# Performance work log

Hardware: AMD Instinct MI355X
Metric: run time of the kernel (lower is better)

Reference implementation:

```python
import jax, jax.numpy as jnp
import numpy as np

NUM_HEADS = 16
HEIGHT = 32
WIDTH = 32
FEATURES_DIM = HEIGHT * WIDTH  # 1024
EMBED_DIM = 1024


def setup_inputs() -> dict:
    key = jax.random.key(0)
    ks = jax.random.split(key, 9)
    s_in = 1.0 / np.sqrt(FEATURES_DIM)
    s_e = 1.0 / np.sqrt(EMBED_DIM)
    return {
        "x": jax.random.normal(ks[0], (16, 512, HEIGHT, WIDTH), dtype=jnp.float32),
        "Wq": jax.random.uniform(ks[1], (EMBED_DIM, FEATURES_DIM), jnp.float32, -s_in, s_in),
        "bq": jax.random.uniform(ks[2], (EMBED_DIM,), jnp.float32, -s_in, s_in),
        "Wk": jax.random.uniform(ks[3], (EMBED_DIM, FEATURES_DIM), jnp.float32, -s_in, s_in),
        "bk": jax.random.uniform(ks[4], (EMBED_DIM,), jnp.float32, -s_in, s_in),
        "Wv": jax.random.uniform(ks[5], (EMBED_DIM, FEATURES_DIM), jnp.float32, -s_in, s_in),
        "bv": jax.random.uniform(ks[6], (EMBED_DIM,), jnp.float32, -s_in, s_in),
        "Wo": jax.random.uniform(ks[7], (FEATURES_DIM, EMBED_DIM), jnp.float32, -s_e, s_e),
        "bo": jax.random.uniform(ks[8], (FEATURES_DIM,), jnp.float32, -s_e, s_e),
    }


def reference(x, Wq, bq, Wk, bk, Wv, bv, Wo, bo):
    B, C, H, W = x.shape
    nh = NUM_HEADS
    hd = EMBED_DIM // nh
    xf = x.reshape(B, C, H * W)  # [B, C, F] - channel tokens
    q = xf @ Wq.T + bq  # [B, C, E]
    k = xf @ Wk.T + bk
    v = xf @ Wv.T + bv
    q = q.reshape(B, C, nh, hd).transpose(0, 2, 1, 3)  # [B, nh, C, hd]
    k = k.reshape(B, C, nh, hd).transpose(0, 2, 1, 3)
    v = v.reshape(B, C, nh, hd).transpose(0, 2, 1, 3)
    scores = jnp.einsum("bhcd,bhkd->bhck", q, k) / jnp.sqrt(jnp.float32(hd))
    attn = jax.nn.softmax(scores, axis=-1)
    out = jnp.einsum("bhck,bhkd->bhcd", attn, v)  # [B, nh, C, hd]
    out = out.transpose(0, 2, 1, 3).reshape(B, C, EMBED_DIM)
    out = out @ Wo.T + bo  # [B, C, F]
    return out.reshape(B, C, H, W)
```

## Files before the change

kernel.cpp:

```cpp
#include <hip/hip_runtime.h>


typedef unsigned short u16;
typedef __attribute__((ext_vector_type(8))) short short8;
typedef __attribute__((ext_vector_type(4))) float f32x4;
typedef __attribute__((ext_vector_type(4))) unsigned short u16x4;

#define MFMA16(a, b, c) __builtin_amdgcn_mfma_f32_16x16x32_bf16(a, b, c, 0, 0, 0)

__device__ __forceinline__ u16 f2bf(float x) {
  unsigned u = __float_as_uint(x);
  u += 0x7FFFu + ((u >> 16) & 1u);
  return (u16)(u >> 16);
}

__device__ __forceinline__ void async16(const void* g, void* l) {
  __builtin_amdgcn_global_load_lds(
      (__attribute__((address_space(1))) unsigned int*)(g),
      (__attribute__((address_space(3))) unsigned int*)(l), 16, 0, 0);
}

__global__ __launch_bounds__(256) void cvt_all(
    const float* __restrict__ x, const float* __restrict__ wq,
    const float* __restrict__ wk, const float* __restrict__ wv,
    const float* __restrict__ wo, u16* __restrict__ dst) {
  int g = blockIdx.x * 256 + threadIdx.x;
  const float* s;
  int off;
  if (g < 2097152) {
    s = x; off = g;
  } else {
    int r = g - 2097152;
    int w = r >> 18;
    off = r & 262143;
    s = (w == 0) ? wq : (w == 1) ? wk : (w == 2) ? wv : wo;
  }
  f32x4 v = ((const f32x4*)s)[off];
  u16x4 o;
#pragma unroll
  for (int j = 0; j < 4; ++j) o[j] = f2bf(v[j]);
  ((u16x4*)dst)[g] = o;
}

__device__ __forceinline__ void gemm8p(const u16* __restrict__ A,
                                       const u16* __restrict__ W, int m0,
                                       int n0, u16* lds, f32x4 acc[8][4]) {
  const int t = threadIdx.x;
  const int wave = t >> 6, lane = t & 63, lr = lane & 15, lg = lane >> 4;
  const int wr = wave >> 2, wn = wave & 3;
  const int srow = t >> 3;
  const int scol = ((t & 7) ^ (srow & 7)) << 3;
  const u16* gA = A + (size_t)(m0 + srow) * 1024 + scol;
  const u16* gB = W + (size_t)(n0 + srow) * 1024 + scol;
  u16* stA = lds + wave * 512;
  u16* stB = lds + 16384 + wave * 512;
  const int arow = (wr * 128 + lr) * 64;
  const int brow = 16384 + (wn * 64 + lr) * 64;
  const int xk = lr & 7;
  const int sw0 = (lg ^ xk) << 3;
  const int sw1 = ((4 + lg) ^ xk) << 3;

#define SA(kt, h)                                                           \
  {                                                                         \
    async16(gA + (2 * (h)) * 65536 + (kt) * 64,                             \
            stA + ((kt) & 1) * 32768 + (2 * (h)) * 4096);                   \
    async16(gA + (2 * (h) + 1) * 65536 + (kt) * 64,                         \
            stA + ((kt) & 1) * 32768 + (2 * (h) + 1) * 4096);               \
  }
#define SB(kt, h)                                                           \
  {                                                                         \
    async16(gB + (2 * (h)) * 65536 + (kt) * 64,                             \
            stB + ((kt) & 1) * 32768 + (2 * (h)) * 4096);                   \
    async16(gB + (2 * (h) + 1) * 65536 + (kt) * 64,                         \
            stB + ((kt) & 1) * 32768 + (2 * (h) + 1) * 4096);               \
  }

  SB(0, 0); SA(0, 0); SB(0, 1); SA(0, 1);
  SB(1, 0); SA(1, 0);
  asm volatile("s_waitcnt vmcnt(4)" ::: "memory");
  __builtin_amdgcn_s_barrier();

  short8 a[8], b[8];
#pragma unroll 2
  for (int tt = 0; tt < 16; ++tt) {
    const u16* bp = lds + (tt & 1) * 32768;
#pragma unroll
    for (int mf = 0; mf < 4; ++mf) {
      a[mf * 2 + 0] = *(const short8*)(bp + arow + mf * 1024 + sw0);
      a[mf * 2 + 1] = *(const short8*)(bp + arow + mf * 1024 + sw1);
    }
#pragma unroll
    for (int nf = 0; nf < 2; ++nf) {
      b[nf * 2 + 0] = *(const short8*)(bp + brow + nf * 1024 + sw0);
      b[nf * 2 + 1] = *(const short8*)(bp + brow + nf * 1024 + sw1);
    }
    if (tt + 1 < 16) SB(tt + 1, 1);
    __builtin_amdgcn_s_barrier();
    asm volatile("s_waitcnt lgkmcnt(0)" ::: "memory");
    __builtin_amdgcn_sched_barrier(0);
    __builtin_amdgcn_s_setprio(1);
#pragma unroll
    for (int mf = 0; mf < 4; ++mf)
#pragma unroll
      for (int nf = 0; nf < 2; ++nf) {
        acc[mf][nf] = MFMA16(a[mf * 2 + 0], b[nf * 2 + 0], acc[mf][nf]);
        acc[mf][nf] = MFMA16(a[mf * 2 + 1], b[nf * 2 + 1], acc[mf][nf]);
      }
    __builtin_amdgcn_s_setprio(0);
    __builtin_amdgcn_s_barrier();
#pragma unroll
    for (int nf = 2; nf < 4; ++nf) {
      b[nf * 2 + 0] = *(const short8*)(bp + brow + nf * 1024 + sw0);
      b[nf * 2 + 1] = *(const short8*)(bp + brow + nf * 1024 + sw1);
    }
    if (tt + 1 < 16) SA(tt + 1, 1);
    __builtin_amdgcn_s_barrier();
    asm volatile("s_waitcnt lgkmcnt(0)" ::: "memory");
    __builtin_amdgcn_sched_barrier(0);
    __builtin_amdgcn_s_setprio(1);
#pragma unroll
    for (int mf = 0; mf < 4; ++mf)
#pragma unroll
      for (int nf = 2; nf < 4; ++nf) {
        acc[mf][nf] = MFMA16(a[mf * 2 + 0], b[nf * 2 + 0], acc[mf][nf]);
        acc[mf][nf] = MFMA16(a[mf * 2 + 1], b[nf * 2 + 1], acc[mf][nf]);
      }
    __builtin_amdgcn_s_setprio(0);
    __builtin_amdgcn_s_barrier();
#pragma unroll
    for (int mf = 4; mf < 8; ++mf) {
      a[(mf - 4) * 2 + 0] = *(const short8*)(bp + arow + mf * 1024 + sw0);
      a[(mf - 4) * 2 + 1] = *(const short8*)(bp + arow + mf * 1024 + sw1);
    }
    if (tt + 2 < 16) SB(tt + 2, 0);
    __builtin_amdgcn_s_barrier();
    asm volatile("s_waitcnt lgkmcnt(0)" ::: "memory");
    __builtin_amdgcn_sched_barrier(0);
    __builtin_amdgcn_s_setprio(1);
#pragma unroll
    for (int mf = 4; mf < 8; ++mf)
#pragma unroll
      for (int nf = 2; nf < 4; ++nf) {
        acc[mf][nf] = MFMA16(a[(mf - 4) * 2 + 0], b[nf * 2 + 0], acc[mf][nf]);
        acc[mf][nf] = MFMA16(a[(mf - 4) * 2 + 1], b[nf * 2 + 1], acc[mf][nf]);
      }
    __builtin_amdgcn_s_setprio(0);
    __builtin_amdgcn_s_barrier();
    if (tt + 2 < 16) SA(tt + 2, 0);
    __builtin_amdgcn_s_setprio(1);
#pragma unroll
    for (int mf = 4; mf < 8; ++mf)
#pragma unroll
      for (int nf = 0; nf < 2; ++nf) {
        acc[mf][nf] = MFMA16(a[(mf - 4) * 2 + 0], b[nf * 2 + 0], acc[mf][nf]);
        acc[mf][nf] = MFMA16(a[(mf - 4) * 2 + 1], b[nf * 2 + 1], acc[mf][nf]);
      }
    __builtin_amdgcn_s_setprio(0);
    if (tt < 14) {
      asm volatile("s_waitcnt vmcnt(4)" ::: "memory");
    } else {
      asm volatile("s_waitcnt vmcnt(0)" ::: "memory");
    }
    __builtin_amdgcn_s_barrier();
  }
#undef SA
#undef SB
}

__global__ __launch_bounds__(512, 2) void gemm_qkv(
    const u16* __restrict__ xb, const u16* __restrict__ w3,
    const float* __restrict__ bq, const float* __restrict__ bk,
    const float* __restrict__ bv, u16* __restrict__ qo, u16* __restrict__ ko,
    u16* __restrict__ vo) {
  __shared__ u16 lds[65536];
  const int id = blockIdx.x;
  const int lid = (id & 7) * 48 + (id >> 3);
  const int tm = lid / 12, tn = lid % 12;
  const int m0 = tm * 256, n0g = tn * 256;
  const int z = n0g >> 10, n0 = n0g & 1023;
  const float* bias = (z == 0) ? bq : (z == 1) ? bk : bv;
  u16* outp = (z == 0) ? qo : (z == 1) ? ko : vo;
  f32x4 acc[8][4];
#pragma unroll
  for (int i = 0; i < 8; ++i)
#pragma unroll
    for (int j = 0; j < 4; ++j) acc[i][j] = (f32x4){0.f, 0.f, 0.f, 0.f};
  gemm8p(xb, w3, m0, n0g, lds, acc);

  const int t = threadIdx.x;
  const int wave = t >> 6, lane = t & 63, lr = lane & 15, lg = lane >> 4;
  const int wr = wave >> 2, wn = wave & 3;
  float bb[4];
#pragma unroll
  for (int nf = 0; nf < 4; ++nf) bb[nf] = bias[n0 + wn * 64 + nf * 16 + lr];
#pragma unroll
  for (int mf = 0; mf < 8; ++mf)
#pragma unroll
    for (int nf = 0; nf < 4; ++nf)
#pragma unroll
      for (int r = 0; r < 4; ++r) {
        int m = m0 + wr * 128 + mf * 16 + lg * 4 + r;
        int n = n0 + wn * 64 + nf * 16 + lr;
        float val = acc[mf][nf][r] + bb[nf];
        int b_ = m >> 9, c = m & 511, h = n >> 6, dd = n & 63;
        int idx = (z == 2) ? ((((b_ << 4) + h) << 15) + (dd << 9) + c)
                           : ((((b_ << 4) + h) << 15) + (c << 6) + dd);
        outp[idx] = f2bf(val);
      }
}

__global__ __launch_bounds__(512, 2) void gemm_oproj(const u16* __restrict__ ab,
                                                     const u16* __restrict__ wo,
                                                     const float* __restrict__ bo,
                                                     float* __restrict__ out) {
  __shared__ u16 lds[65536];
  const int id = blockIdx.x;
  const int lid = (id & 7) * 16 + (id >> 3);
  const int m0 = (lid >> 2) * 256, n0 = (lid & 3) * 256;
  f32x4 acc[8][4];
#pragma unroll
  for (int i = 0; i < 8; ++i)
#pragma unroll
    for (int j = 0; j < 4; ++j) acc[i][j] = (f32x4){0.f, 0.f, 0.f, 0.f};
  gemm8p(ab, wo, m0, n0, lds, acc);

  const int t = threadIdx.x;
  const int wave = t >> 6, lane = t & 63, lr = lane & 15, lg = lane >> 4;
  const int wr = wave >> 2, wn = wave & 3;
  float bb[4];
#pragma unroll
  for (int nf = 0; nf < 4; ++nf) bb[nf] = bo[n0 + wn * 64 + nf * 16 + lr];
#pragma unroll
  for (int mf = 0; mf < 8; ++mf)
#pragma unroll
    for (int nf = 0; nf < 4; ++nf)
#pragma unroll
      for (int r = 0; r < 4; ++r) {
        int m = m0 + wr * 128 + mf * 16 + lg * 4 + r;
        int n = n0 + wn * 64 + nf * 16 + lr;
        out[m * 1024 + n] = acc[mf][nf][r] + bb[nf];
      }
}

__global__ __launch_bounds__(512, 2) void attn_kernel(
    const u16* __restrict__ qb, const u16* __restrict__ kb,
    const u16* __restrict__ vb, u16* __restrict__ ab) {
  __shared__ u16 lK[32768];
  __shared__ u16 lV[32768];
  __shared__ u16 lP[8192];
  const int t = threadIdx.x;
  const int bh = blockIdx.x;
  const int b_ = bh >> 4, h_ = bh & 15;
  const u16* kg = kb + bh * 32768;
  const u16* vg = vb + bh * 32768;
#pragma unroll
  for (int i = 0; i < 8; ++i) {
    int row = i * 64 + (t >> 3), slot = t & 7;
    short8 kv = *(const short8*)(kg + row * 64 + slot * 8);
    *(short8*)(lK + row * 64 + ((slot ^ (row & 7)) << 3)) = kv;
    int vrow = i * 8 + (t >> 6), vslot = t & 63;
    short8 vv = *(const short8*)(vg + vrow * 512 + vslot * 8);
    *(short8*)(lV + vrow * 512 + ((vslot ^ (vrow & 7)) << 3)) = vv;
  }

  const int wv_ = t >> 6, lane = t & 63, lr = lane & 15, lg = lane >> 4;
  u16* lPw = lP + wv_ * 1024;
  const u16* qg = qb + bh * 32768;
  const float sc = 0.125f * 1.44269504088896f;

  short8 a0q[4], a1q[4];
#pragma unroll
  for (int qi = 0; qi < 4; ++qi) {
    const int qrow = (wv_ * 4 + qi) * 16;
    a0q[qi] = *(const short8*)(qg + (qrow + lr) * 64 + lg * 8);
    a1q[qi] = *(const short8*)(qg + (qrow + lr) * 64 + 32 + lg * 8);
  }
  __syncthreads();

#pragma unroll 1
  for (int qi = 0; qi < 4; ++qi) {
    const int qrow = (wv_ * 4 + qi) * 16;
    f32x4 s[32];
    __builtin_amdgcn_s_setprio(1);
#pragma unroll
    for (int f = 0; f < 32; ++f) {
      const u16* kr = lK + (f * 16 + lr) * 64;
      short8 k0 = *(const short8*)(kr + ((lg ^ (lr & 7)) << 3));
      short8 k1 = *(const short8*)(kr + (((4 + lg) ^ (lr & 7)) << 3));
      f32x4 z4 = (f32x4){0.f, 0.f, 0.f, 0.f};
      z4 = MFMA16(a0q[qi], k0, z4);
      z4 = MFMA16(a1q[qi], k1, z4);
      s[f] = z4;
    }
    __builtin_amdgcn_s_setprio(0);
    float inv[4];
#pragma unroll
    for (int r = 0; r < 4; ++r) {
      float m_ = s[0][r];
#pragma unroll
      for (int f = 1; f < 32; ++f) m_ = fmaxf(m_, s[f][r]);
      m_ = fmaxf(m_, __shfl_xor(m_, 1));
      m_ = fmaxf(m_, __shfl_xor(m_, 2));
      m_ = fmaxf(m_, __shfl_xor(m_, 4));
      m_ = fmaxf(m_, __shfl_xor(m_, 8));
      float sm = 0.f;
#pragma unroll
      for (int f = 0; f < 32; ++f) {
        float e = exp2f((s[f][r] - m_) * sc);
        s[f][r] = e;
        sm += e;
      }
      sm += __shfl_xor(sm, 1);
      sm += __shfl_xor(sm, 2);
      sm += __shfl_xor(sm, 4);
      sm += __shfl_xor(sm, 8);
      inv[r] = 1.f / sm;
    }
    f32x4 o[4];
#pragma unroll
    for (int i = 0; i < 4; ++i) o[i] = (f32x4){0.f, 0.f, 0.f, 0.f};
#pragma unroll
    for (int ch = 0; ch < 8; ++ch) {
#pragma unroll
      for (int cf = 0; cf < 4; ++cf)
#pragma unroll
        for (int r = 0; r < 4; ++r) {
          int q = lg * 4 + r, kc = cf * 16 + lr;
          lPw[q * 64 + (((kc >> 3) ^ (q & 7)) << 3) + (kc & 7)] =
              f2bf(s[ch * 4 + cf][r]);
        }
      asm volatile("s_waitcnt lgkmcnt(0)" ::: "memory");
      const u16* pr = lPw + lr * 64;
      short8 pa0 = *(const short8*)(pr + ((lg ^ (lr & 7)) << 3));
      short8 pa1 = *(const short8*)(pr + (((4 + lg) ^ (lr & 7)) << 3));
      __builtin_amdgcn_s_setprio(1);
#pragma unroll
      for (int df = 0; df < 4; ++df) {
        const u16* vr = lV + (df * 16 + lr) * 512;
        short8 v0 = *(const short8*)(vr + (((ch * 8 + lg) ^ (lr & 7)) << 3));
        short8 v1 =
            *(const short8*)(vr + (((ch * 8 + 4 + lg) ^ (lr & 7)) << 3));
        o[df] = MFMA16(pa0, v0, o[df]);
        o[df] = MFMA16(pa1, v1, o[df]);
      }
      __builtin_amdgcn_s_setprio(0);
    }
#pragma unroll
    for (int df = 0; df < 4; ++df)
#pragma unroll
      for (int r = 0; r < 4; ++r) {
        int q = qrow + lg * 4 + r, dd = df * 16 + lr;
        ab[(b_ * 512 + q) * 1024 + h_ * 64 + dd] = f2bf(o[df][r] * inv[r]);
      }
  }
}

extern "C" void kernel_launch(void* const* d_in, const int* in_sizes, int n_in,
                              void* d_out, int out_size, void* d_ws,
                              size_t ws_size, hipStream_t stream) {
  (void)in_sizes; (void)n_in; (void)out_size;
  const float* x  = (const float*)d_in[0];
  const float* Wq = (const float*)d_in[1];
  const float* bq = (const float*)d_in[2];
  const float* Wk = (const float*)d_in[3];
  const float* bk = (const float*)d_in[4];
  const float* Wv = (const float*)d_in[5];
  const float* bv = (const float*)d_in[6];
  const float* Wo = (const float*)d_in[7];
  const float* bo = (const float*)d_in[8];
  float* out = (float*)d_out;

  if (ws_size < 75497472u) return;
  u16* xb  = (u16*)d_ws;
  u16* w3b = xb + 8388608;
  u16* wob = w3b + 3145728;
  u16* qbuf = wob + 1048576;
  u16* kbuf = qbuf + 8388608;
  u16* vbuf = kbuf + 8388608;
  u16* abuf = xb;

  cvt_all<<<12288, 256, 0, stream>>>(x, Wq, Wk, Wv, Wo, xb);
  gemm_qkv<<<384, 512, 0, stream>>>(xb, w3b, bq, bk, bv, qbuf, kbuf, vbuf);
  attn_kernel<<<256, 512, 0, stream>>>(qbuf, kbuf, vbuf, abuf);
  gemm_oproj<<<128, 512, 0, stream>>>(abuf, wob, bo, out);
}
```

Measured before the change: 186.3 us.

## Split output projection into 256x128 tiles and simplify attention Q loading

```diff
diff --git a/kernel.cpp b/kernel.cpp
--- a/kernel.cpp
+++ b/kernel.cpp
@@ -167,6 +167,93 @@
 #undef SB
 }
 
+__device__ __forceinline__ void gemm2x(const u16* __restrict__ A,
+                                       const u16* __restrict__ W, int m0,
+                                       int n0, u16* lds, f32x4 acc[8][2]) {
+  const int t = threadIdx.x;
+  const int wave = t >> 6, lane = t & 63, lr = lane & 15, lg = lane >> 4;
+  const int wr = wave >> 2, wn = wave & 3;
+  const int srow = t >> 3;
+  const int scol = ((t & 7) ^ (srow & 7)) << 3;
+  const u16* gA = A + (size_t)(m0 + srow) * 1024 + scol;
+  const u16* gB = W + (size_t)(n0 + srow) * 1024 + scol;
+  u16* stA = lds + wave * 512;
+  u16* stB = lds + 16384 + wave * 512;
+  const int arow = (wr * 128 + lr) * 64;
+  const int brow = 16384 + (wn * 32 + lr) * 64;
+  const int xk = lr & 7;
+  const int sw0 = (lg ^ xk) << 3;
+  const int sw1 = ((4 + lg) ^ xk) << 3;
+
+#define SA2(kt)                                                              \
+  {                                                                          \
+    async16(gA + 0 * 65536 + (kt) * 64, stA + ((kt) & 1) * 24576 + 0 * 4096); \
+    async16(gA + 1 * 65536 + (kt) * 64, stA + ((kt) & 1) * 24576 + 1 * 4096); \
+    async16(gA + 2 * 65536 + (kt) * 64, stA + ((kt) & 1) * 24576 + 2 * 4096); \
+    async16(gA + 3 * 65536 + (kt) * 64, stA + ((kt) & 1) * 24576 + 3 * 4096); \
+  }
+#define SB2(kt)                                                              \
+  {                                                                          \
+    async16(gB + 0 * 65536 + (kt) * 64, stB + ((kt) & 1) * 24576 + 0 * 4096); \
+    async16(gB + 1 * 65536 + (kt) * 64, stB + ((kt) & 1) * 24576 + 1 * 4096); \
+  }
+
+  SA2(0); SB2(0);
+  asm volatile("s_waitcnt vmcnt(0)" ::: "memory");
+  __builtin_amdgcn_s_barrier();
+
+  short8 a[8], b[4];
+#pragma unroll 2
+  for (int tt = 0; tt < 16; ++tt) {
+    const u16* bp = lds + (tt & 1) * 24576;
+#pragma unroll
+    for (int mf = 0; mf < 4; ++mf) {
+      a[mf * 2 + 0] = *(const short8*)(bp + arow + mf * 1024 + sw0);
+      a[mf * 2 + 1] = *(const short8*)(bp + arow + mf * 1024 + sw1);
+    }
+#pragma unroll
+    for (int nf = 0; nf < 2; ++nf) {
+      b[nf * 2 + 0] = *(const short8*)(bp + brow + nf * 1024 + sw0);
+      b[nf * 2 + 1] = *(const short8*)(bp + brow + nf * 1024 + sw1);
+    }
+    if (tt + 1 < 16) { SA2(tt + 1); SB2(tt + 1); }
+    __builtin_amdgcn_s_barrier();
+    asm volatile("s_waitcnt lgkmcnt(0)" ::: "memory");
+    __builtin_amdgcn_sched_barrier(0);
+    __builtin_amdgcn_s_setprio(1);
+#pragma unroll
+    for (int mf = 0; mf < 4; ++mf)
+#pragma unroll
+      for (int nf = 0; nf < 2; ++nf) {
+        acc[mf][nf] = MFMA16(a[mf * 2 + 0], b[nf * 2 + 0], acc[mf][nf]);
+        acc[mf][nf] = MFMA16(a[mf * 2 + 1], b[nf * 2 + 1], acc[mf][nf]);
+      }
+    __builtin_amdgcn_s_setprio(0);
+    __builtin_amdgcn_s_barrier();
+#pragma unroll
+    for (int mf = 4; mf < 8; ++mf) {
+      a[(mf - 4) * 2 + 0] = *(const short8*)(bp + arow + mf * 1024 + sw0);
+      a[(mf - 4) * 2 + 1] = *(const short8*)(bp + arow + mf * 1024 + sw1);
+    }
+    __builtin_amdgcn_s_barrier();
+    asm volatile("s_waitcnt lgkmcnt(0)" ::: "memory");
+    __builtin_amdgcn_sched_barrier(0);
+    __builtin_amdgcn_s_setprio(1);
+#pragma unroll
+    for (int mf = 4; mf < 8; ++mf)
+#pragma unroll
+      for (int nf = 0; nf < 2; ++nf) {
+        acc[mf][nf] = MFMA16(a[(mf - 4) * 2 + 0], b[nf * 2 + 0], acc[mf][nf]);
+        acc[mf][nf] = MFMA16(a[(mf - 4) * 2 + 1], b[nf * 2 + 1], acc[mf][nf]);
+      }
+    __builtin_amdgcn_s_setprio(0);
+    asm volatile("s_waitcnt vmcnt(0)" ::: "memory");
+    __builtin_amdgcn_s_barrier();
+  }
+#undef SA2
+#undef SB2
+}
+
 __global__ __launch_bounds__(512, 2) void gemm_qkv(
     const u16* __restrict__ xb, const u16* __restrict__ w3,
     const float* __restrict__ bq, const float* __restrict__ bk,
@@ -209,35 +296,35 @@
       }
 }
 
-__global__ __launch_bounds__(512, 2) void gemm_oproj(const u16* __restrict__ ab,
+__global__ __launch_bounds__(512, 1) void gemm_oproj(const u16* __restrict__ ab,
                                                      const u16* __restrict__ wo,
                                                      const float* __restrict__ bo,
                                                      float* __restrict__ out) {
-  __shared__ u16 lds[65536];
+  __shared__ u16 lds[49152];
   const int id = blockIdx.x;
-  const int lid = (id & 7) * 16 + (id >> 3);
-  const int m0 = (lid >> 2) * 256, n0 = (lid & 3) * 256;
-  f32x4 acc[8][4];
+  const int lid = (id & 7) * 32 + (id >> 3);
+  const int m0 = (lid >> 3) * 256, n0 = (lid & 7) * 128;
+  f32x4 acc[8][2];
 #pragma unroll
   for (int i = 0; i < 8; ++i)
 #pragma unroll
-    for (int j = 0; j < 4; ++j) acc[i][j] = (f32x4){0.f, 0.f, 0.f, 0.f};
-  gemm8p(ab, wo, m0, n0, lds, acc);
+    for (int j = 0; j < 2; ++j) acc[i][j] = (f32x4){0.f, 0.f, 0.f, 0.f};
+  gemm2x(ab, wo, m0, n0, lds, acc);
 
   const int t = threadIdx.x;
   const int wave = t >> 6, lane = t & 63, lr = lane & 15, lg = lane >> 4;
   const int wr = wave >> 2, wn = wave & 3;
-  float bb[4];
-#pragma unroll
-  for (int nf = 0; nf < 4; ++nf) bb[nf] = bo[n0 + wn * 64 + nf * 16 + lr];
+  float bb[2];
+#pragma unroll
+  for (int nf = 0; nf < 2; ++nf) bb[nf] = bo[n0 + wn * 32 + nf * 16 + lr];
 #pragma unroll
   for (int mf = 0; mf < 8; ++mf)
 #pragma unroll
-    for (int nf = 0; nf < 4; ++nf)
+    for (int nf = 0; nf < 2; ++nf)
 #pragma unroll
       for (int r = 0; r < 4; ++r) {
         int m = m0 + wr * 128 + mf * 16 + lg * 4 + r;
-        int n = n0 + wn * 64 + nf * 16 + lr;
+        int n = n0 + wn * 32 + nf * 16 + lr;
         out[m * 1024 + n] = acc[mf][nf][r] + bb[nf];
       }
 }
@@ -262,37 +349,29 @@
     short8 vv = *(const short8*)(vg + vrow * 512 + vslot * 8);
     *(short8*)(lV + vrow * 512 + ((vslot ^ (vrow & 7)) << 3)) = vv;
   }
+  __syncthreads();
 
   const int wv_ = t >> 6, lane = t & 63, lr = lane & 15, lg = lane >> 4;
   u16* lPw = lP + wv_ * 1024;
   const u16* qg = qb + bh * 32768;
   const float sc = 0.125f * 1.44269504088896f;
 
-  short8 a0q[4], a1q[4];
-#pragma unroll
-  for (int qi = 0; qi < 4; ++qi) {
-    const int qrow = (wv_ * 4 + qi) * 16;
-    a0q[qi] = *(const short8*)(qg + (qrow + lr) * 64 + lg * 8);
-    a1q[qi] = *(const short8*)(qg + (qrow + lr) * 64 + 32 + lg * 8);
-  }
-  __syncthreads();
-
 #pragma unroll 1
   for (int qi = 0; qi < 4; ++qi) {
     const int qrow = (wv_ * 4 + qi) * 16;
+    short8 a0 = *(const short8*)(qg + (qrow + lr) * 64 + lg * 8);
+    short8 a1 = *(const short8*)(qg + (qrow + lr) * 64 + 32 + lg * 8);
     f32x4 s[32];
-    __builtin_amdgcn_s_setprio(1);
 #pragma unroll
     for (int f = 0; f < 32; ++f) {
       const u16* kr = lK + (f * 16 + lr) * 64;
       short8 k0 = *(const short8*)(kr + ((lg ^ (lr & 7)) << 3));
       short8 k1 = *(const short8*)(kr + (((4 + lg) ^ (lr & 7)) << 3));
       f32x4 z4 = (f32x4){0.f, 0.f, 0.f, 0.f};
-      z4 = MFMA16(a0q[qi], k0, z4);
-      z4 = MFMA16(a1q[qi], k1, z4);
+      z4 = MFMA16(a0, k0, z4);
+      z4 = MFMA16(a1, k1, z4);
       s[f] = z4;
     }
-    __builtin_amdgcn_s_setprio(0);
     float inv[4];
 #pragma unroll
     for (int r = 0; r < 4; ++r) {
@@ -333,7 +412,6 @@
       const u16* pr = lPw + lr * 64;
       short8 pa0 = *(const short8*)(pr + ((lg ^ (lr & 7)) << 3));
       short8 pa1 = *(const short8*)(pr + (((4 + lg) ^ (lr & 7)) << 3));
-      __builtin_amdgcn_s_setprio(1);
 #pragma unroll
       for (int df = 0; df < 4; ++df) {
         const u16* vr = lV + (df * 16 + lr) * 512;
@@ -343,7 +421,6 @@
         o[df] = MFMA16(pa0, v0, o[df]);
         o[df] = MFMA16(pa1, v1, o[df]);
       }
-      __builtin_amdgcn_s_setprio(0);
     }
 #pragma unroll
     for (int df = 0; df < 4; ++df)
@@ -382,5 +459,5 @@
   cvt_all<<<12288, 256, 0, stream>>>(x, Wq, Wk, Wv, Wo, xb);
   gemm_qkv<<<384, 512, 0, stream>>>(xb, w3b, bq, bk, bv, qbuf, kbuf, vbuf);
   attn_kernel<<<256, 512, 0, stream>>>(qbuf, kbuf, vbuf, abuf);
-  gemm_oproj<<<128, 512, 0, stream>>>(abuf, wob, bo, out);
-}
+  gemm_oproj<<<256, 512, 0, stream>>>(abuf, wob, bo, out);
+}
```

Result: faster. 168.2 us (median of 2 runs) (-9.7%).
